# Kernel tuning notes

Hardware: AMD Instinct MI355X
Metric: run time of the kernel (lower is better)

Reference implementation:

```python
import jax, jax.numpy as jnp
import numpy as np

B, H, N = 256, 128, 2048

def setup_inputs() -> dict:
    key = jax.random.key(0)
    k1, k2, k3, k4, k5 = jax.random.split(key, 5)
    return {
        "static_hidden": jax.random.normal(k1, (B, H, N), dtype=jnp.float32),
        "dynamic_hidden": jax.random.normal(k2, (B, H, N), dtype=jnp.float32),
        "decoder_hidden": jax.random.normal(k3, (B, H), dtype=jnp.float32),
        "v": jax.random.normal(k4, (1, 1, H), dtype=jnp.float32) * 0.05,
        "W": jax.random.normal(k5, (1, H, 3 * H), dtype=jnp.float32) * 0.05,
    }

def reference(static_hidden, dynamic_hidden, decoder_hidden, v, W):
    # hidden: [B, 3H, N] = concat(static, dynamic, broadcast(decoder))
    dec = jnp.broadcast_to(decoder_hidden[:, :, None], static_hidden.shape)
    hidden = jnp.concatenate((static_hidden, dynamic_hidden, dec), axis=1)
    # W @ hidden: [B, H, N]; tanh; v @ .: [B, 1, N]
    Wh = jnp.tanh(jnp.einsum('hk,bkn->bhn', W[0], hidden))
    scores = jnp.einsum('h,bhn->bn', v[0, 0], Wh)[:, None, :]  # [B,1,N]
    return jax.nn.softmax(scores, axis=2)
```

## Files before the change

### kernel.cpp

```cpp
#include <hip/hip_runtime.h>
#include <cstddef>

#define Bn 256
#define Hd 128
#define Nd 2048
#define K3 384
#define K2 256

typedef _Float16 half8 __attribute__((ext_vector_type(8)));
typedef float    float4v __attribute__((ext_vector_type(4)));

__device__ __forceinline__ float fast_tanh(float x) {
    return 1.0f - __fdividef(2.0f, __expf(2.0f * x) + 1.0f);
}

__global__ void prep_w16(const float* __restrict__ W, _Float16* __restrict__ Wf) {
    int idx = blockIdx.x * 256 + threadIdx.x;
    int h = idx >> 8, k = idx & 255;
    Wf[idx] = (_Float16)W[h * K3 + k];
}

__global__ void prep_c(const float* __restrict__ W, const float* __restrict__ dec,
                       float* __restrict__ cb) {
    __shared__ float dl[Hd];
    int b = blockIdx.x;
    int h = threadIdx.x;
    dl[h] = dec[b * Hd + h];
    __syncthreads();
    float acc = 0.f;
    #pragma unroll 8
    for (int k = 0; k < Hd; ++k)
        acc = fmaf(W[h * K3 + 256 + k], dl[k], acc);
    cb[b * Hd + h] = acc;
}

__global__ __launch_bounds__(512, 8)
void score_kernel(const float* __restrict__ shp, const float* __restrict__ dhp,
                  const _Float16* __restrict__ Wf, const float* __restrict__ cbp,
                  const float* __restrict__ v, float* __restrict__ out) {
    __shared__ __align__(16) _Float16 xl[64 * 256];
    __shared__ float red[4 * 64];

    const int tid  = threadIdx.x;
    const int w    = __builtin_amdgcn_readfirstlane(tid >> 6);
    const int lane = tid & 63;
    const int qd   = lane >> 4;
    const int ln   = lane & 15;
    const int b    = blockIdx.y;
    const int n0   = blockIdx.x * 64;

    {
        const int nq = lane & 15;
        const int kh = lane >> 4;
        const int n  = 4 * nq;
        const int kb = 8 * kh;
        const float* base = (w < 4)
            ? shp + (size_t)b * (Hd * (size_t)Nd) + (size_t)(32 * w + kb) * Nd + n0 + n
            : dhp + (size_t)b * (Hd * (size_t)Nd) + (size_t)(32 * (w - 4) + kb) * Nd + n0 + n;

        float4v xv[8];
        #pragma unroll
        for (int j = 0; j < 8; ++j)
            xv[j] = *reinterpret_cast<const float4v*>(base + (size_t)j * Nd);

        const int ck = 4 * w + kh;
        #pragma unroll
        for (int r = 0; r < 4; ++r) {
            half8 e;
            #pragma unroll
            for (int j = 0; j < 8; ++j) e[j] = (_Float16)xv[j][r];
            const int row = n + r;
            const int p = ck ^ ((row >> 1) & 7);
            *reinterpret_cast<half8*>(&xl[row * 256 + p * 8]) = e;
        }
    }
    __syncthreads();

    const int mh = w & 3;
    const int nh = w >> 2;
    const int h0 = mh * 32;
    const int swr = (ln >> 1) & 7;

    float4v acc[2][2];
    #pragma unroll
    for (int Mt = 0; Mt < 2; ++Mt) {
        float4v c4 = *reinterpret_cast<const float4v*>(cbp + b * Hd + h0 + Mt * 16 + qd * 4);
        #pragma unroll
        for (int Nt = 0; Nt < 2; ++Nt) acc[Mt][Nt] = c4;
    }

    const _Float16* wp0 = Wf + ((h0 + ln) << 8) + qd * 8;
    const _Float16* wp1 = Wf + ((h0 + 16 + ln) << 8) + qd * 8;
    half8 a0 = *reinterpret_cast<const half8*>(wp0);
    half8 a1 = *reinterpret_cast<const half8*>(wp1);
    #pragma unroll
    for (int kt = 0; kt < 8; ++kt) {
        half8 a0n, a1n;
        if (kt < 7) {
            a0n = *reinterpret_cast<const half8*>(wp0 + (kt + 1) * 32);
            a1n = *reinterpret_cast<const half8*>(wp1 + (kt + 1) * 32);
        }
        half8 Bf[2];
        const int ckb = kt * 4 + qd;
        #pragma unroll
        for (int Nt = 0; Nt < 2; ++Nt) {
            const int row = nh * 32 + Nt * 16 + ln;
            Bf[Nt] = *reinterpret_cast<const half8*>(&xl[row * 256 + ((ckb ^ swr) << 3)]);
        }
        #pragma unroll
        for (int Nt = 0; Nt < 2; ++Nt) {
            acc[0][Nt] = __builtin_amdgcn_mfma_f32_16x16x32_f16(a0, Bf[Nt], acc[0][Nt], 0, 0, 0);
            acc[1][Nt] = __builtin_amdgcn_mfma_f32_16x16x32_f16(a1, Bf[Nt], acc[1][Nt], 0, 0, 0);
        }
        if (kt < 7) { a0 = a0n; a1 = a1n; }
    }

    float4v v0 = *reinterpret_cast<const float4v*>(v + h0 + qd * 4);
    float4v v1 = *reinterpret_cast<const float4v*>(v + h0 + 16 + qd * 4);
    #pragma unroll
    for (int Nt = 0; Nt < 2; ++Nt) {
        float part = 0.f;
        #pragma unroll
        for (int r = 0; r < 4; ++r) {
            part = fmaf(v0[r], fast_tanh(acc[0][Nt][r]), part);
            part = fmaf(v1[r], fast_tanh(acc[1][Nt][r]), part);
        }
        part += __shfl_xor(part, 16);
        part += __shfl_xor(part, 32);
        if (qd == 0) red[mh * 64 + nh * 32 + Nt * 16 + ln] = part;
    }
    __syncthreads();
    if (tid < 64) {
        float s = red[tid] + red[64 + tid] + red[128 + tid] + red[192 + tid];
        out[(size_t)b * Nd + n0 + tid] = s;
    }
}

__global__ void softmax_k(float* __restrict__ out) {
    int b = blockIdx.x;
    float* row = out + (size_t)b * Nd;
    int tid = threadIdx.x;

    float loc[8];
    float mx = -3.4e38f;
    #pragma unroll
    for (int i = 0; i < 8; ++i) {
        loc[i] = row[tid + (i << 8)];
        mx = fmaxf(mx, loc[i]);
    }
    #pragma unroll
    for (int off = 32; off > 0; off >>= 1) mx = fmaxf(mx, __shfl_xor(mx, off));
    __shared__ float s4[4];
    if ((tid & 63) == 0) s4[tid >> 6] = mx;
    __syncthreads();
    mx = fmaxf(fmaxf(s4[0], s4[1]), fmaxf(s4[2], s4[3]));

    float sum = 0.f;
    #pragma unroll
    for (int i = 0; i < 8; ++i) {
        loc[i] = __expf(loc[i] - mx);
        sum += loc[i];
    }
    #pragma unroll
    for (int off = 32; off > 0; off >>= 1) sum += __shfl_xor(sum, off);
    __shared__ float s4b[4];
    if ((tid & 63) == 0) s4b[tid >> 6] = sum;
    __syncthreads();
    sum = s4b[0] + s4b[1] + s4b[2] + s4b[3];

    float inv = 1.0f / sum;
    #pragma unroll
    for (int i = 0; i < 8; ++i) row[tid + (i << 8)] = loc[i] * inv;
}

extern "C" void kernel_launch(void* const* d_in, const int* in_sizes, int n_in,
                              void* d_out, int out_size, void* d_ws, size_t ws_size,
                              hipStream_t stream) {
    const float* shp = (const float*)d_in[0];
    const float* dhp = (const float*)d_in[1];
    const float* dec = (const float*)d_in[2];
    const float* v   = (const float*)d_in[3];
    const float* W   = (const float*)d_in[4];
    float* out = (float*)d_out;

    _Float16* Wf = (_Float16*)d_ws;
    float* cbp = (float*)((char*)d_ws + 65536);

    hipLaunchKernelGGL(prep_w16, dim3(128), dim3(256), 0, stream, W, Wf);
    hipLaunchKernelGGL(prep_c,   dim3(Bn),  dim3(Hd),  0, stream, W, dec, cbp);
    hipLaunchKernelGGL(score_kernel, dim3(Nd / 64, Bn), dim3(512), 0, stream,
                       shp, dhp, Wf, cbp, v, out);
    hipLaunchKernelGGL(softmax_k, dim3(Bn), dim3(256), 0, stream, out);
}
```

Before: 573.8 us.

## Stage inputs via global_load_lds DMA and halve the N tile to 32

The input tile is now loaded straight into LDS as raw fp32 using global_load_lds 16-byte DMA. A separate pass then converts it to swizzled fp16, replacing the old path that loaded into registers, converted, and stored. The N tile shrinks from 64 to 32 columns per block, which doubles the block count and gives each wave one 16-column MFMA tile instead of two. The aim is to cut VGPR pressure and latency on this memory-bound streaming kernel. In exchange the block needs more LDS, adds an extra barrier, and reuses the W fragments less.

```diff
diff --git a/kernel.cpp b/kernel.cpp
--- a/kernel.cpp
+++ b/kernel.cpp
@@ -1,17 +1,26 @@
 #include <hip/hip_runtime.h>
 #include <cstddef>
+#include <cstdint>
 
 #define Bn 256
 #define Hd 128
 #define Nd 2048
 #define K3 384
-#define K2 256
+#define NT 32
 
 typedef _Float16 half8 __attribute__((ext_vector_type(8)));
 typedef float    float4v __attribute__((ext_vector_type(4)));
+typedef unsigned int u32;
 
 __device__ __forceinline__ float fast_tanh(float x) {
     return 1.0f - __fdividef(2.0f, __expf(2.0f * x) + 1.0f);
+}
+
+__device__ __forceinline__ void dma16(const float* g, const void* l) {
+    __builtin_amdgcn_global_load_lds(
+        (const __attribute__((address_space(1))) u32*)(uintptr_t)g,
+        (__attribute__((address_space(3))) u32*)(u32)(uintptr_t)l,
+        16, 0, 0);
 }
 
 __global__ void prep_w16(const float* __restrict__ W, _Float16* __restrict__ Wf) {
@@ -34,12 +43,13 @@
     cb[b * Hd + h] = acc;
 }
 
-__global__ __launch_bounds__(512, 8)
+__global__ __launch_bounds__(512, 6)
 void score_kernel(const float* __restrict__ shp, const float* __restrict__ dhp,
                   const _Float16* __restrict__ Wf, const float* __restrict__ cbp,
                   const float* __restrict__ v, float* __restrict__ out) {
-    __shared__ __align__(16) _Float16 xl[64 * 256];
-    __shared__ float red[4 * 64];
+    __shared__ __align__(16) float    xraw[256 * NT];
+    __shared__ __align__(16) _Float16 xl[NT * 256];
+    __shared__ float red[4 * NT];
 
     const int tid  = threadIdx.x;
     const int w    = __builtin_amdgcn_readfirstlane(tid >> 6);
@@ -47,47 +57,44 @@
     const int qd   = lane >> 4;
     const int ln   = lane & 15;
     const int b    = blockIdx.y;
-    const int n0   = blockIdx.x * 64;
+    const int n0   = blockIdx.x * NT;
 
     {
-        const int nq = lane & 15;
-        const int kh = lane >> 4;
-        const int n  = 4 * nq;
-        const int kb = 8 * kh;
-        const float* base = (w < 4)
-            ? shp + (size_t)b * (Hd * (size_t)Nd) + (size_t)(32 * w + kb) * Nd + n0 + n
-            : dhp + (size_t)b * (Hd * (size_t)Nd) + (size_t)(32 * (w - 4) + kb) * Nd + n0 + n;
+        const float* arr = (w < 4) ? shp : dhp;
+        const int kr = (w < 4) ? 32 * w : 32 * w - 128;
+        const float* gb = arr + (size_t)b * (Hd * (size_t)Nd) + (size_t)kr * Nd
+                        + (size_t)(lane >> 3) * Nd + n0 + 4 * (lane & 7);
+        #pragma unroll
+        for (int t = 0; t < 4; ++t)
+            dma16(gb + (size_t)(8 * t) * Nd,
+                  (const char*)xraw + (32 * w + 8 * t) * (NT * 4));
+    }
+    __syncthreads();
 
-        float4v xv[8];
+    {
+        const int n   = tid & 31;
+        const int s   = n & 7;
+        const int kc0 = tid >> 5;
         #pragma unroll
-        for (int j = 0; j < 8; ++j)
-            xv[j] = *reinterpret_cast<const float4v*>(base + (size_t)j * Nd);
-
-        const int ck = 4 * w + kh;
-        #pragma unroll
-        for (int r = 0; r < 4; ++r) {
+        for (int u = 0; u < 2; ++u) {
+            const int kc = kc0 + 16 * u;
             half8 e;
             #pragma unroll
-            for (int j = 0; j < 8; ++j) e[j] = (_Float16)xv[j][r];
-            const int row = n + r;
-            const int p = ck ^ ((row >> 1) & 7);
-            *reinterpret_cast<half8*>(&xl[row * 256 + p * 8]) = e;
+            for (int j = 0; j < 8; ++j)
+                e[j] = (_Float16)xraw[(kc * 8 + j) * NT + n];
+            *reinterpret_cast<half8*>(&xl[n * 256 + ((kc ^ s) << 3)]) = e;
         }
     }
     __syncthreads();
 
-    const int mh = w & 3;
-    const int nh = w >> 2;
-    const int h0 = mh * 32;
-    const int swr = (ln >> 1) & 7;
+    const int mh  = w & 3;
+    const int nh  = w >> 2;
+    const int h0  = mh * 32;
+    const int row = nh * 16 + ln;
+    const int sw  = row & 7;
 
-    float4v acc[2][2];
-    #pragma unroll
-    for (int Mt = 0; Mt < 2; ++Mt) {
-        float4v c4 = *reinterpret_cast<const float4v*>(cbp + b * Hd + h0 + Mt * 16 + qd * 4);
-        #pragma unroll
-        for (int Nt = 0; Nt < 2; ++Nt) acc[Mt][Nt] = c4;
-    }
+    float4v acc0 = *reinterpret_cast<const float4v*>(cbp + b * Hd + h0 + qd * 4);
+    float4v acc1 = *reinterpret_cast<const float4v*>(cbp + b * Hd + h0 + 16 + qd * 4);
 
     const _Float16* wp0 = Wf + ((h0 + ln) << 8) + qd * 8;
     const _Float16* wp1 = Wf + ((h0 + 16 + ln) << 8) + qd * 8;
@@ -100,38 +107,27 @@
             a0n = *reinterpret_cast<const half8*>(wp0 + (kt + 1) * 32);
             a1n = *reinterpret_cast<const half8*>(wp1 + (kt + 1) * 32);
         }
-        half8 Bf[2];
-        const int ckb = kt * 4 + qd;
-        #pragma unroll
-        for (int Nt = 0; Nt < 2; ++Nt) {
-            const int row = nh * 32 + Nt * 16 + ln;
-            Bf[Nt] = *reinterpret_cast<const half8*>(&xl[row * 256 + ((ckb ^ swr) << 3)]);
-        }
-        #pragma unroll
-        for (int Nt = 0; Nt < 2; ++Nt) {
-            acc[0][Nt] = __builtin_amdgcn_mfma_f32_16x16x32_f16(a0, Bf[Nt], acc[0][Nt], 0, 0, 0);
-            acc[1][Nt] = __builtin_amdgcn_mfma_f32_16x16x32_f16(a1, Bf[Nt], acc[1][Nt], 0, 0, 0);
-        }
+        const int ck = kt * 4 + qd;
+        half8 Bf = *reinterpret_cast<const half8*>(&xl[row * 256 + ((ck ^ sw) << 3)]);
+        acc0 = __builtin_amdgcn_mfma_f32_16x16x32_f16(a0, Bf, acc0, 0, 0, 0);
+        acc1 = __builtin_amdgcn_mfma_f32_16x16x32_f16(a1, Bf, acc1, 0, 0, 0);
         if (kt < 7) { a0 = a0n; a1 = a1n; }
     }
 
     float4v v0 = *reinterpret_cast<const float4v*>(v + h0 + qd * 4);
     float4v v1 = *reinterpret_cast<const float4v*>(v + h0 + 16 + qd * 4);
+    float part = 0.f;
     #pragma unroll
-    for (int Nt = 0; Nt < 2; ++Nt) {
-        float part = 0.f;
-        #pragma unroll
-        for (int r = 0; r < 4; ++r) {
-            part = fmaf(v0[r], fast_tanh(acc[0][Nt][r]), part);
-            part = fmaf(v1[r], fast_tanh(acc[1][Nt][r]), part);
-        }
-        part += __shfl_xor(part, 16);
-        part += __shfl_xor(part, 32);
-        if (qd == 0) red[mh * 64 + nh * 32 + Nt * 16 + ln] = part;
+    for (int r = 0; r < 4; ++r) {
+        part = fmaf(v0[r], fast_tanh(acc0[r]), part);
+        part = fmaf(v1[r], fast_tanh(acc1[r]), part);
     }
+    part += __shfl_xor(part, 16);
+    part += __shfl_xor(part, 32);
+    if (qd == 0) red[mh * 32 + row] = part;
     __syncthreads();
-    if (tid < 64) {
-        float s = red[tid] + red[64 + tid] + red[128 + tid] + red[192 + tid];
+    if (tid < NT) {
+        float s = red[tid] + red[32 + tid] + red[64 + tid] + red[96 + tid];
         out[(size_t)b * Nd + n0 + tid] = s;
     }
 }
@@ -188,7 +184,7 @@
 
     hipLaunchKernelGGL(prep_w16, dim3(128), dim3(256), 0, stream, W, Wf);
     hipLaunchKernelGGL(prep_c,   dim3(Bn),  dim3(Hd),  0, stream, W, dec, cbp);
-    hipLaunchKernelGGL(score_kernel, dim3(Nd / 64, Bn), dim3(512), 0, stream,
+    hipLaunchKernelGGL(score_kernel, dim3(Nd / NT, Bn), dim3(512), 0, stream,
                        shp, dhp, Wf, cbp, v, out);
     hipLaunchKernelGGL(softmax_k, dim3(Bn), dim3(256), 0, stream, out);
 }
```

Measured after the change: 696.6 us. 1.21x slower.

## Warp-specialize score kernel with double-buffered producer/consumer tiles over batches

Applied to the files above, without the earlier changes.

Restructures the score kernel into a persistent-style block that loops over 16 batches per 128-column tile. Four waves act as producers, loading and converting the fp32 activations to fp16 into alternating shared-memory buffers. The other four waves run MFMA over all 128 hidden rows and write scores directly, dropping the cross-wave reduction. The aim is to overlap global loads with compute and reuse W fragments across iterations. In exchange the grid shrinks to 256 blocks with large LDS use (128 KB) and low occupancy, and only half the waves issue loads.

```diff
diff --git a/kernel.cpp b/kernel.cpp
--- a/kernel.cpp
+++ b/kernel.cpp
@@ -1,11 +1,13 @@
 #include <hip/hip_runtime.h>
 #include <cstddef>
+#include <cstdint>
 
 #define Bn 256
 #define Hd 128
 #define Nd 2048
 #define K3 384
-#define K2 256
+#define NTILE 128
+#define BPC 16
 
 typedef _Float16 half8 __attribute__((ext_vector_type(8)));
 typedef float    float4v __attribute__((ext_vector_type(4)));
@@ -34,105 +36,145 @@
     cb[b * Hd + h] = acc;
 }
 
-__global__ __launch_bounds__(512, 8)
+__global__ __launch_bounds__(512, 2)
 void score_kernel(const float* __restrict__ shp, const float* __restrict__ dhp,
                   const _Float16* __restrict__ Wf, const float* __restrict__ cbp,
                   const float* __restrict__ v, float* __restrict__ out) {
-    __shared__ __align__(16) _Float16 xl[64 * 256];
-    __shared__ float red[4 * 64];
+    __shared__ __align__(16) _Float16 xl0[NTILE * 256];
+    __shared__ __align__(16) _Float16 xl1[NTILE * 256];
 
     const int tid  = threadIdx.x;
     const int w    = __builtin_amdgcn_readfirstlane(tid >> 6);
     const int lane = tid & 63;
     const int qd   = lane >> 4;
     const int ln   = lane & 15;
-    const int b    = blockIdx.y;
-    const int n0   = blockIdx.x * 64;
-
-    {
-        const int nq = lane & 15;
-        const int kh = lane >> 4;
-        const int n  = 4 * nq;
-        const int kb = 8 * kh;
-        const float* base = (w < 4)
-            ? shp + (size_t)b * (Hd * (size_t)Nd) + (size_t)(32 * w + kb) * Nd + n0 + n
-            : dhp + (size_t)b * (Hd * (size_t)Nd) + (size_t)(32 * (w - 4) + kb) * Nd + n0 + n;
-
-        float4v xv[8];
+    const int bid  = blockIdx.x;
+    const int n0   = (bid & 15) * NTILE;
+    const int b0   = (bid >> 4) * BPC;
+    const size_t bstr = (size_t)Hd * Nd;
+
+    if (w < 4) {
+        const float* arr = (w < 2) ? shp : dhp;
+        const int    kb  = (w & 1) * 64;
+        const int    nc  = lane & 31;
+        const int    hi  = lane >> 5;
+        const float* gb  = arr + (size_t)b0 * bstr
+                         + (size_t)(kb + 8 * hi) * Nd + n0 + 4 * nc;
+
         #pragma unroll
-        for (int j = 0; j < 8; ++j)
-            xv[j] = *reinterpret_cast<const float4v*>(base + (size_t)j * Nd);
-
-        const int ck = 4 * w + kh;
+        for (int c2 = 0; c2 < 4; ++c2) {
+            const float* src = gb + (size_t)(16 * c2) * Nd;
+            float4v xv[8];
+            #pragma unroll
+            for (int j = 0; j < 8; ++j)
+                xv[j] = *reinterpret_cast<const float4v*>(src + (size_t)j * Nd);
+            const int ck = 8 * w + 2 * c2 + hi;
+            #pragma unroll
+            for (int r = 0; r < 4; ++r) {
+                half8 e;
+                #pragma unroll
+                for (int j = 0; j < 8; ++j) e[j] = (_Float16)xv[j][r];
+                const int n = 4 * nc + r;
+                *reinterpret_cast<half8*>(&xl0[n * 256 + ((ck ^ ((n >> 1) & 7)) << 3)]) = e;
+            }
+        }
+        __syncthreads();
+
+        for (int it = 0; it < BPC; ++it) {
+            if (it + 1 < BPC) {
+                _Float16* buf = ((it + 1) & 1) ? xl1 : xl0;
+                const float* gt = gb + (size_t)(it + 1) * bstr;
+                #pragma unroll
+                for (int c2 = 0; c2 < 4; ++c2) {
+                    const float* src = gt + (size_t)(16 * c2) * Nd;
+                    float4v xv[8];
+                    #pragma unroll
+                    for (int j = 0; j < 8; ++j)
+                        xv[j] = *reinterpret_cast<const float4v*>(src + (size_t)j * Nd);
+                    const int ck = 8 * w + 2 * c2 + hi;
+                    #pragma unroll
+                    for (int r = 0; r < 4; ++r) {
+                        half8 e;
+                        #pragma unroll
+                        for (int j = 0; j < 8; ++j) e[j] = (_Float16)xv[j][r];
+                        const int n = 4 * nc + r;
+                        *reinterpret_cast<half8*>(&buf[n * 256 + ((ck ^ ((n >> 1) & 7)) << 3)]) = e;
+                    }
+                }
+            }
+            __syncthreads();
+        }
+    } else {
+        const int cw = w & 3;
+
+        float4v vv[8];
         #pragma unroll
-        for (int r = 0; r < 4; ++r) {
-            half8 e;
-            #pragma unroll
-            for (int j = 0; j < 8; ++j) e[j] = (_Float16)xv[j][r];
-            const int row = n + r;
-            const int p = ck ^ ((row >> 1) & 7);
-            *reinterpret_cast<half8*>(&xl[row * 256 + p * 8]) = e;
+        for (int Mt = 0; Mt < 8; ++Mt)
+            vv[Mt] = *reinterpret_cast<const float4v*>(v + Mt * 16 + qd * 4);
+
+        __syncthreads();
+
+        for (int it = 0; it < BPC; ++it) {
+            const _Float16* buf = (it & 1) ? xl1 : xl0;
+            const int b = b0 + it;
+
+            float4v acc[8][2];
+            #pragma unroll
+            for (int Mt = 0; Mt < 8; ++Mt) {
+                float4v c4 = *reinterpret_cast<const float4v*>(
+                    cbp + (size_t)b * Hd + Mt * 16 + qd * 4);
+                acc[Mt][0] = c4;
+                acc[Mt][1] = c4;
+            }
+
+            half8 a[8], an[8];
+            #pragma unroll
+            for (int Mt = 0; Mt < 8; ++Mt)
+                a[Mt] = *reinterpret_cast<const half8*>(Wf + ((Mt * 16 + ln) << 8) + qd * 8);
+
+            #pragma unroll
+            for (int kt = 0; kt < 8; ++kt) {
+                if (kt < 7) {
+                    #pragma unroll
+                    for (int Mt = 0; Mt < 8; ++Mt)
+                        an[Mt] = *reinterpret_cast<const half8*>(
+                            Wf + ((Mt * 16 + ln) << 8) + (kt + 1) * 32 + qd * 8);
+                }
+                half8 Bf[2];
+                const int ckb = kt * 4 + qd;
+                #pragma unroll
+                for (int Nt = 0; Nt < 2; ++Nt) {
+                    const int row = cw * 32 + Nt * 16 + ln;
+                    Bf[Nt] = *reinterpret_cast<const half8*>(
+                        &buf[row * 256 + ((ckb ^ ((row >> 1) & 7)) << 3)]);
+                }
+                #pragma unroll
+                for (int Mt = 0; Mt < 8; ++Mt) {
+                    acc[Mt][0] = __builtin_amdgcn_mfma_f32_16x16x32_f16(a[Mt], Bf[0], acc[Mt][0], 0, 0, 0);
+                    acc[Mt][1] = __builtin_amdgcn_mfma_f32_16x16x32_f16(a[Mt], Bf[1], acc[Mt][1], 0, 0, 0);
+                }
+                if (kt < 7) {
+                    #pragma unroll
+                    for (int Mt = 0; Mt < 8; ++Mt) a[Mt] = an[Mt];
+                }
+            }
+
+            #pragma unroll
+            for (int Nt = 0; Nt < 2; ++Nt) {
+                float part = 0.f;
+                #pragma unroll
+                for (int Mt = 0; Mt < 8; ++Mt) {
+                    #pragma unroll
+                    for (int r = 0; r < 4; ++r)
+                        part = fmaf(vv[Mt][r], fast_tanh(acc[Mt][Nt][r]), part);
+                }
+                part += __shfl_xor(part, 16);
+                part += __shfl_xor(part, 32);
+                if (qd == 0)
+                    out[(size_t)b * Nd + n0 + cw * 32 + Nt * 16 + ln] = part;
+            }
+            __syncthreads();
         }
-    }
-    __syncthreads();
-
-    const int mh = w & 3;
-    const int nh = w >> 2;
-    const int h0 = mh * 32;
-    const int swr = (ln >> 1) & 7;
-
-    float4v acc[2][2];
-    #pragma unroll
-    for (int Mt = 0; Mt < 2; ++Mt) {
-        float4v c4 = *reinterpret_cast<const float4v*>(cbp + b * Hd + h0 + Mt * 16 + qd * 4);
-        #pragma unroll
-        for (int Nt = 0; Nt < 2; ++Nt) acc[Mt][Nt] = c4;
-    }
-
-    const _Float16* wp0 = Wf + ((h0 + ln) << 8) + qd * 8;
-    const _Float16* wp1 = Wf + ((h0 + 16 + ln) << 8) + qd * 8;
-    half8 a0 = *reinterpret_cast<const half8*>(wp0);
-    half8 a1 = *reinterpret_cast<const half8*>(wp1);
-    #pragma unroll
-    for (int kt = 0; kt < 8; ++kt) {
-        half8 a0n, a1n;
-        if (kt < 7) {
-            a0n = *reinterpret_cast<const half8*>(wp0 + (kt + 1) * 32);
-            a1n = *reinterpret_cast<const half8*>(wp1 + (kt + 1) * 32);
-        }
-        half8 Bf[2];
-        const int ckb = kt * 4 + qd;
-        #pragma unroll
-        for (int Nt = 0; Nt < 2; ++Nt) {
-            const int row = nh * 32 + Nt * 16 + ln;
-            Bf[Nt] = *reinterpret_cast<const half8*>(&xl[row * 256 + ((ckb ^ swr) << 3)]);
-        }
-        #pragma unroll
-        for (int Nt = 0; Nt < 2; ++Nt) {
-            acc[0][Nt] = __builtin_amdgcn_mfma_f32_16x16x32_f16(a0, Bf[Nt], acc[0][Nt], 0, 0, 0);
-            acc[1][Nt] = __builtin_amdgcn_mfma_f32_16x16x32_f16(a1, Bf[Nt], acc[1][Nt], 0, 0, 0);
-        }
-        if (kt < 7) { a0 = a0n; a1 = a1n; }
-    }
-
-    float4v v0 = *reinterpret_cast<const float4v*>(v + h0 + qd * 4);
-    float4v v1 = *reinterpret_cast<const float4v*>(v + h0 + 16 + qd * 4);
-    #pragma unroll
-    for (int Nt = 0; Nt < 2; ++Nt) {
-        float part = 0.f;
-        #pragma unroll
-        for (int r = 0; r < 4; ++r) {
-            part = fmaf(v0[r], fast_tanh(acc[0][Nt][r]), part);
-            part = fmaf(v1[r], fast_tanh(acc[1][Nt][r]), part);
-        }
-        part += __shfl_xor(part, 16);
-        part += __shfl_xor(part, 32);
-        if (qd == 0) red[mh * 64 + nh * 32 + Nt * 16 + ln] = part;
-    }
-    __syncthreads();
-    if (tid < 64) {
-        float s = red[tid] + red[64 + tid] + red[128 + tid] + red[192 + tid];
-        out[(size_t)b * Nd + n0 + tid] = s;
     }
 }
 
@@ -188,7 +230,7 @@
 
     hipLaunchKernelGGL(prep_w16, dim3(128), dim3(256), 0, stream, W, Wf);
     hipLaunchKernelGGL(prep_c,   dim3(Bn),  dim3(Hd),  0, stream, W, dec, cbp);
-    hipLaunchKernelGGL(score_kernel, dim3(Nd / 64, Bn), dim3(512), 0, stream,
+    hipLaunchKernelGGL(score_kernel, dim3((Nd / NTILE) * (Bn / BPC)), dim3(512), 0, stream,
                        shp, dhp, Wf, cbp, v, out);
     hipLaunchKernelGGL(softmax_k, dim3(Bn), dim3(256), 0, stream, out);
 }
```

New measurement: 712.9 us. 24.2% more time.
